# Kernel optimization log

Hardware: AMD Instinct MI355X
Metric: run time of the kernel (lower is better)

The kernel has to match this reference:

```python
import jax, jax.numpy as jnp
import numpy as np

N_NODES = 10000
IN_SIZE, H_SIZE, OUT_SIZE = 512, 512, 64
N_EDGES = 163840


def gcn_conv(x, edge_index, W, b, n_nodes):
    """PyG-style GCNConv: add self-loops, sym-normalize, x @ W, scatter-add, + bias."""
    src, dst = edge_index[0], edge_index[1]
    loop = jnp.arange(n_nodes, dtype=src.dtype)
    src = jnp.concatenate([src, loop])
    dst = jnp.concatenate([dst, loop])
    # degree over destinations (self-loops included)
    deg = jax.ops.segment_sum(jnp.ones_like(dst, dtype=x.dtype), dst, num_segments=n_nodes)
    dinv = jnp.where(deg > 0, jax.lax.rsqrt(deg), 0.0)
    norm = dinv[src] * dinv[dst]                      # [E+N]
    h = x @ W                                          # [N, out]
    msg = h[src] * norm[:, None]                       # gather + scale
    out = jax.ops.segment_sum(msg, dst, num_segments=n_nodes)  # scatter-add
    return out + b


def setup_inputs() -> dict:
    key = jax.random.key(0)
    k = jax.random.split(key, 6)
    x = jax.random.normal(k[0], (N_NODES, IN_SIZE), dtype=jnp.float32)
    edge_index = jax.random.randint(k[1], (2, N_EDGES), 0, N_NODES, dtype=jnp.int64 if jax.config.read('jax_enable_x64') else jnp.int32)
    # Glorot-ish init for weights, zero bias (PyG default)
    W1 = jax.random.normal(k[2], (IN_SIZE, H_SIZE), dtype=jnp.float32) * (1.0 / np.sqrt(IN_SIZE))
    b1 = jnp.zeros((H_SIZE,), dtype=jnp.float32)
    W2 = jax.random.normal(k[3], (H_SIZE, OUT_SIZE), dtype=jnp.float32) * (1.0 / np.sqrt(H_SIZE))
    b2 = jnp.zeros((OUT_SIZE,), dtype=jnp.float32)
    return {"x": x, "edge_index": edge_index, "W1": W1, "b1": b1, "W2": W2, "b2": b2}


def reference(x, edge_index, W1, b1, W2, b2):
    n = x.shape[0]
    h = gcn_conv(x, edge_index, W1, b1, n)
    h = jax.nn.relu(h)
    h = gcn_conv(h, edge_index, W2, b2, n)
    return (h, jax.nn.log_softmax(h, axis=1))
```

## Files before the change

kernel.cpp:

```cpp
#include <hip/hip_runtime.h>
#include <math.h>

#define NN 10000
#define INF 512
#define HF  512
#define OF  64
#define NE  163840
#define MAXDEG 64

typedef __attribute__((ext_vector_type(8))) short bf16x8_t;
typedef __attribute__((ext_vector_type(4))) float f32x4_t;

__device__ inline ushort f2bf(float f) {
    unsigned u = __float_as_uint(f);
    u = (u + 0x7FFF + ((u >> 16) & 1)) >> 16;
    return (ushort)u;
}
__device__ inline float bf2f(ushort u) {
    return __uint_as_float(((unsigned)u) << 16);
}

#define GLL(gp, lp) __builtin_amdgcn_global_load_lds(                         \
    (const __attribute__((address_space(1))) unsigned int*)(gp),              \
    (__attribute__((address_space(3))) unsigned int*)(lp), 16, 0, 0)

#define CCB_X  2500
#define CCB_W1 2756
#define CCB_W2 2788
#define CCB_Z  2828
__global__ __launch_bounds__(256) void k_cvt(const float* __restrict__ X,
                                             ushort* __restrict__ Xb,
                                             const float* __restrict__ W1,
                                             ushort* __restrict__ W1T,
                                             const float* __restrict__ W2,
                                             ushort* __restrict__ W2T,
                                             int* __restrict__ gdeg) {
    __shared__ float tl[32][33];
    int b = blockIdx.x, t = threadIdx.x;
    if (b < CCB_X) {
        int i = (b * 256 + t) * 2;
        const float4* Xv = (const float4*)X;
        float4 v0 = Xv[i], v1 = Xv[i + 1];
        ushort4 o0, o1;
        o0.x = f2bf(v0.x); o0.y = f2bf(v0.y); o0.z = f2bf(v0.z); o0.w = f2bf(v0.w);
        o1.x = f2bf(v1.x); o1.y = f2bf(v1.y); o1.z = f2bf(v1.z); o1.w = f2bf(v1.w);
        ((ushort4*)Xb)[i] = o0;
        ((ushort4*)Xb)[i + 1] = o1;
    } else if (b < CCB_W2) {
        const float* W; ushort* WT; int N, tile;
        if (b < CCB_W1) { W = W1; WT = W1T; N = 512; tile = b - CCB_X; }
        else            { W = W2; WT = W2T; N = 64;  tile = b - CCB_W1; }
        int k0 = (tile & 15) * 32;
        int n0 = (tile >> 4) * 32;
        int tx = t & 31, ty = t >> 5;
#pragma unroll
        for (int i = 0; i < 4; i++)
            tl[ty + i * 8][tx] = W[(size_t)(k0 + ty + i * 8) * N + n0 + tx];
        __syncthreads();
#pragma unroll
        for (int i = 0; i < 4; i++)
            WT[(size_t)(n0 + ty + i * 8) * 512 + k0 + tx] = f2bf(tl[tx][ty + i * 8]);
    } else {
        int i = (b - CCB_W2) * 256 + t;
        if (i < NN) gdeg[i] = 0;
    }
}

#define GEMM_B 316
__global__ __launch_bounds__(256) void k_gemm_ell(const ushort* __restrict__ Xb,
                                                  const ushort* __restrict__ WT,
                                                  ushort* __restrict__ Y,
                                                  const int* __restrict__ src,
                                                  const int* __restrict__ dst,
                                                  int* __restrict__ gdeg,
                                                  int* __restrict__ ell, int E) {
    __shared__ ushort As[128 * 64];
    __shared__ ushort Bs[128 * 64];
    int b = blockIdx.x;
    int tid = threadIdx.x;
    if (b >= GEMM_B) {
        int e = (b - GEMM_B) * 256 + tid;
        if (e < E) {
            int s = src[e], d = dst[e];
            int r = atomicAdd(&gdeg[d], 1);
            if (r < MAXDEG) ell[d * MAXDEG + r] = s;
        }
        return;
    }
    int lane = tid & 63;
    int wave = tid >> 6;
    int m = lane & 15;
    int q = lane >> 4;
    int m7 = m & 7;
    int wr = wave >> 1;
    int wc = wave & 1;
    int row0 = (b % 79) * 128;
    int col0 = (b / 79) * 128;

    int lrow = lane >> 3;
    int lg = ((lane & 7) ^ lrow) * 8;

    f32x4_t acc[4][4];
#pragma unroll
    for (int r = 0; r < 4; r++)
#pragma unroll
        for (int c = 0; c < 4; c++) acc[r][c] = (f32x4_t){0.f, 0.f, 0.f, 0.f};

    const ushort* gA0 = Xb + (size_t)(row0 + wave * 32 + lrow) * 512 + lg;
    const ushort* gB0 = WT + (size_t)(col0 + wave * 32 + lrow) * 512 + lg;
    ushort* lA0 = As + (wave * 32) * 64;
    ushort* lB0 = Bs + (wave * 32) * 64;

    for (int kb = 0; kb < 512; kb += 64) {
#pragma unroll
        for (int j = 0; j < 4; j++) {
            GLL(gA0 + kb + j * 8 * 512, lA0 + j * 8 * 64);
            GLL(gB0 + kb + j * 8 * 512, lB0 + j * 8 * 64);
        }
        __syncthreads();
#pragma unroll
        for (int kc = 0; kc < 2; kc++) {
            bf16x8_t a[4], bb[4];
            int slot = ((kc * 4 + q) ^ m7) * 8;
#pragma unroll
            for (int r = 0; r < 4; r++)
                a[r] = *(const bf16x8_t*)(As + (wr * 64 + r * 16 + m) * 64 + slot);
#pragma unroll
            for (int c = 0; c < 4; c++)
                bb[c] = *(const bf16x8_t*)(Bs + (wc * 64 + c * 16 + m) * 64 + slot);
#pragma unroll
            for (int r = 0; r < 4; r++)
#pragma unroll
                for (int c = 0; c < 4; c++)
                    acc[r][c] = __builtin_amdgcn_mfma_f32_16x16x32_bf16(a[r], bb[c], acc[r][c], 0, 0, 0);
        }
        __syncthreads();
    }
#pragma unroll
    for (int r = 0; r < 4; r++) {
#pragma unroll
        for (int c = 0; c < 4; c++) {
#pragma unroll
            for (int reg = 0; reg < 4; reg++) {
                int row = row0 + wr * 64 + r * 16 + q * 4 + reg;
                int col = col0 + wc * 64 + c * 16 + m;
                if (row < NN) Y[(size_t)row * 512 + col] = f2bf(acc[r][c][reg]);
            }
        }
    }
}

__global__ __launch_bounds__(256) void k_gemm64_mfma(const ushort* __restrict__ Ab,
                                                     const ushort* __restrict__ W2T,
                                                     ushort* __restrict__ Y) {
    __shared__ ushort As[64 * 64];
    __shared__ ushort Bs[64 * 64];
    int tid = threadIdx.x;
    int lane = tid & 63;
    int wave = tid >> 6;
    int m = lane & 15;
    int q = lane >> 4;
    int m7 = m & 7;
    int row0 = blockIdx.x * 64;

    int lrow = lane >> 3;
    int lg = ((lane & 7) ^ lrow) * 8;

    f32x4_t acc[4];
#pragma unroll
    for (int c = 0; c < 4; c++) acc[c] = (f32x4_t){0.f, 0.f, 0.f, 0.f};

    const ushort* gA0 = Ab + (size_t)(row0 + wave * 16 + lrow) * 512 + lg;
    const ushort* gB0 = W2T + (size_t)(wave * 16 + lrow) * 512 + lg;
    ushort* lA0 = As + (wave * 16) * 64;
    ushort* lB0 = Bs + (wave * 16) * 64;

    for (int kb = 0; kb < 512; kb += 64) {
#pragma unroll
        for (int j = 0; j < 2; j++) {
            GLL(gA0 + kb + j * 8 * 512, lA0 + j * 8 * 64);
            GLL(gB0 + kb + j * 8 * 512, lB0 + j * 8 * 64);
        }
        __syncthreads();
#pragma unroll
        for (int kc = 0; kc < 2; kc++) {
            int slot = ((kc * 4 + q) ^ m7) * 8;
            bf16x8_t a = *(const bf16x8_t*)(As + (wave * 16 + m) * 64 + slot);
#pragma unroll
            for (int c = 0; c < 4; c++) {
                bf16x8_t bfr = *(const bf16x8_t*)(Bs + (c * 16 + m) * 64 + slot);
                acc[c] = __builtin_amdgcn_mfma_f32_16x16x32_bf16(a, bfr, acc[c], 0, 0, 0);
            }
        }
        __syncthreads();
    }
#pragma unroll
    for (int c = 0; c < 4; c++) {
#pragma unroll
        for (int reg = 0; reg < 4; reg++) {
            int row = row0 + wave * 16 + q * 4 + reg;
            int col = c * 16 + m;
            if (row < NN) Y[(size_t)row * 64 + col] = f2bf(acc[c][reg]);
        }
    }
}

__global__ __launch_bounds__(64) void k_agg1(const ushort* __restrict__ h1b,
                                             const int* __restrict__ gdeg,
                                             const int* __restrict__ ell,
                                             const float* __restrict__ b,
                                             ushort* __restrict__ a1b) {
    __shared__ int   sidx[64];
    __shared__ float swt[64];
    int bid = blockIdx.x;
    int slice = bid & 3;
    int v = bid >> 2;
    int t = threadIdx.x;
    int fb = slice * 128 + t * 2;
    int deg = gdeg[v]; if (deg > MAXDEG) deg = MAXDEG;
    float dv = rsqrtf((float)(deg + 1));
    int s = 0; float wt = 0.f;
    if (t < deg) {
        s = ell[v * MAXDEG + t];
        wt = rsqrtf((float)(gdeg[s] + 1)) * dv;
    }
    sidx[t] = s; swt[t] = wt;
    __syncthreads();

    float ax[8], ay[8];
#pragma unroll
    for (int k = 0; k < 8; k++) { ax[k] = 0.f; ay[k] = 0.f; }
    {
        ushort2 u = *(const ushort2*)(h1b + (size_t)v * 512 + fb);
        float dv2 = dv * dv;
        ax[0] = bf2f(u.x) * dv2;
        ay[0] = bf2f(u.y) * dv2;
    }
    int nr = (deg + 7) & ~7;
    for (int i = 0; i < nr; i += 8) {
        int   sK[8]; float wK[8];
#pragma unroll
        for (int k = 0; k < 8; k++) { sK[k] = sidx[i + k]; wK[k] = swt[i + k]; }
#pragma unroll
        for (int k = 0; k < 8; k++) {
            ushort2 u = *(const ushort2*)(h1b + (size_t)sK[k] * 512 + fb);
            ax[k] += bf2f(u.x) * wK[k];
            ay[k] += bf2f(u.y) * wK[k];
        }
    }
    float tx = ((ax[0] + ax[1]) + (ax[2] + ax[3])) + ((ax[4] + ax[5]) + (ax[6] + ax[7]));
    float ty = ((ay[0] + ay[1]) + (ay[2] + ay[3])) + ((ay[4] + ay[5]) + (ay[6] + ay[7]));
    tx += b[fb];
    ty += b[fb + 1];
    ushort2 o;
    o.x = f2bf(tx > 0.f ? tx : 0.f);
    o.y = f2bf(ty > 0.f ? ty : 0.f);
    *(ushort2*)(a1b + (size_t)v * 512 + fb) = o;
}

__global__ __launch_bounds__(64) void k_agg2_lsm(const ushort* __restrict__ h2b,
                                                 const int* __restrict__ gdeg,
                                                 const int* __restrict__ ell,
                                                 const float* __restrict__ b,
                                                 float* __restrict__ out) {
    __shared__ int   sidx[64];
    __shared__ float swt[64];
    int v = blockIdx.x;
    int t = threadIdx.x;
    int deg = gdeg[v]; if (deg > MAXDEG) deg = MAXDEG;
    float dv = rsqrtf((float)(deg + 1));
    int s = 0; float wt = 0.f;
    if (t < deg) {
        s = ell[v * MAXDEG + t];
        wt = rsqrtf((float)(gdeg[s] + 1)) * dv;
    }
    sidx[t] = s; swt[t] = wt;
    __syncthreads();

    float acc[8];
#pragma unroll
    for (int k = 0; k < 8; k++) acc[k] = 0.f;
    acc[0] = bf2f(h2b[(size_t)v * 64 + t]) * (dv * dv);

    int nr = (deg + 7) & ~7;
    for (int i = 0; i < nr; i += 8) {
        int   sK[8]; float wK[8];
#pragma unroll
        for (int k = 0; k < 8; k++) { sK[k] = sidx[i + k]; wK[k] = swt[i + k]; }
#pragma unroll
        for (int k = 0; k < 8; k++)
            acc[k] += bf2f(h2b[(size_t)sK[k] * 64 + t]) * wK[k];
    }
    float h = ((acc[0] + acc[1]) + (acc[2] + acc[3])) +
              ((acc[4] + acc[5]) + (acc[6] + acc[7]));
    h += b[t];
    out[(size_t)v * 64 + t] = h;
    float m = h;
#pragma unroll
    for (int off = 32; off >= 1; off >>= 1) m = fmaxf(m, __shfl_xor(m, off, 64));
    float e = expf(h - m);
    float ssum = e;
#pragma unroll
    for (int off = 32; off >= 1; off >>= 1) ssum += __shfl_xor(ssum, off, 64);
    out[(size_t)NN * OF + (size_t)v * 64 + t] = h - m - logf(ssum);
}


extern "C" void kernel_launch(void* const* d_in, const int* in_sizes, int n_in,
                              void* d_out, int out_size, void* d_ws, size_t ws_size,
                              hipStream_t stream) {
    const float* x  = (const float*)d_in[0];
    const int*   ei = (const int*)d_in[1];
    const float* W1 = (const float*)d_in[2];
    const float* b1 = (const float*)d_in[3];
    const float* W2 = (const float*)d_in[4];
    const float* b2 = (const float*)d_in[5];
    float* out = (float*)d_out;

    int E = in_sizes[1] / 2;
    const int* src = ei;
    const int* dst = ei + E;

    char* w = (char*)d_ws;
    auto carve = [&](size_t bytes) {
        char* p = w;
        w += (bytes + 255) & ~size_t(255);
        return p;
    };
    ushort* Xb     = (ushort*)carve((size_t)NN * 512 * 2);
    ushort* h1b    = (ushort*)carve((size_t)NN * 512 * 2);
    ushort* a1b    = (ushort*)carve((size_t)NN * 512 * 2);
    ushort* h2b    = (ushort*)carve((size_t)NN * 64 * 2);
    ushort* W1Tb   = (ushort*)carve((size_t)512 * 512 * 2);
    ushort* W2Tb   = (ushort*)carve((size_t)64 * 512 * 2);
    int*   gdeg    = (int*)carve((size_t)NN * 4);
    int*   ell     = (int*)carve((size_t)NN * MAXDEG * 4);
    (void)ws_size;

    int fillB = (E + 255) / 256;
    k_cvt<<<CCB_Z, 256, 0, stream>>>(x, Xb, W1, W1Tb, W2, W2Tb, gdeg);
    k_gemm_ell<<<GEMM_B + fillB, 256, 0, stream>>>(Xb, W1Tb, h1b, src, dst,
                                                   gdeg, ell, E);
    k_agg1<<<NN * 4, 64, 0, stream>>>(h1b, gdeg, ell, b1, a1b);
    k_gemm64_mfma<<<(NN + 63) / 64, 256, 0, stream>>>(a1b, W2Tb, h2b);
    k_agg2_lsm<<<NN, 64, 0, stream>>>(h2b, gdeg, ell, b2, out);
}
```

Baseline: 131.4 us.

## Fuse layer-1 aggregation with layer-2 GEMM using split-K atomic accumulation

Replaces the separate agg1 and 64-wide GEMM kernels with one kernel. Each block gathers and aggregates 128 nodes over a 128-feature slice into LDS, applies bias and ReLU, then multiplies by the matching W2 slice with MFMA. The four slice partials are combined through fp32 atomicAdd into a buffer zeroed in the conversion kernel. This removes the a1 round trip through global memory and one launch. In exchange the gather runs on only 316 blocks with serial per-wave node loops, which reduces latency hiding, and layer-2 aggregation now reads fp32 instead of bf16.

```diff
diff --git a/kernel.cpp b/kernel.cpp
--- a/kernel.cpp
+++ b/kernel.cpp
@@ -28,13 +28,15 @@
 #define CCB_W1 2756
 #define CCB_W2 2788
 #define CCB_Z  2828
+#define CCB_H2 3453
 __global__ __launch_bounds__(256) void k_cvt(const float* __restrict__ X,
                                              ushort* __restrict__ Xb,
                                              const float* __restrict__ W1,
                                              ushort* __restrict__ W1T,
                                              const float* __restrict__ W2,
                                              ushort* __restrict__ W2T,
-                                             int* __restrict__ gdeg) {
+                                             int* __restrict__ gdeg,
+                                             float* __restrict__ h2f) {
     __shared__ float tl[32][33];
     int b = blockIdx.x, t = threadIdx.x;
     if (b < CCB_X) {
@@ -60,9 +62,12 @@
 #pragma unroll
         for (int i = 0; i < 4; i++)
             WT[(size_t)(n0 + ty + i * 8) * 512 + k0 + tx] = f2bf(tl[tx][ty + i * 8]);
-    } else {
+    } else if (b < CCB_Z) {
         int i = (b - CCB_W2) * 256 + t;
         if (i < NN) gdeg[i] = 0;
+    } else {
+        int i = (b - CCB_Z) * 256 + t;
+        ((float4*)h2f)[i] = make_float4(0.f, 0.f, 0.f, 0.f);
     }
 }
 
@@ -150,115 +155,115 @@
     }
 }
 
-__global__ __launch_bounds__(256) void k_gemm64_mfma(const ushort* __restrict__ Ab,
-                                                     const ushort* __restrict__ W2T,
-                                                     ushort* __restrict__ Y) {
-    __shared__ ushort As[64 * 64];
-    __shared__ ushort Bs[64 * 64];
+#define FUSE_B 316
+#define LDA2 136
+__global__ __launch_bounds__(256) void k_fuse(const ushort* __restrict__ h1b,
+                                              const int* __restrict__ gdeg,
+                                              const int* __restrict__ ell,
+                                              const float* __restrict__ b1,
+                                              const ushort* __restrict__ W2T,
+                                              float* __restrict__ h2f) {
+    __shared__ ushort a1s[128 * LDA2];
+    __shared__ ushort w2s[64 * LDA2];
+    int bid = blockIdx.x;
+    int slice = bid & 3;
+    int nt = bid >> 2;
     int tid = threadIdx.x;
     int lane = tid & 63;
-    int wave = tid >> 6;
-    int m = lane & 15;
-    int q = lane >> 4;
-    int m7 = m & 7;
-    int row0 = blockIdx.x * 64;
-
-    int lrow = lane >> 3;
-    int lg = ((lane & 7) ^ lrow) * 8;
-
-    f32x4_t acc[4];
-#pragma unroll
-    for (int c = 0; c < 4; c++) acc[c] = (f32x4_t){0.f, 0.f, 0.f, 0.f};
-
-    const ushort* gA0 = Ab + (size_t)(row0 + wave * 16 + lrow) * 512 + lg;
-    const ushort* gB0 = W2T + (size_t)(wave * 16 + lrow) * 512 + lg;
-    ushort* lA0 = As + (wave * 16) * 64;
-    ushort* lB0 = Bs + (wave * 16) * 64;
-
-    for (int kb = 0; kb < 512; kb += 64) {
-#pragma unroll
-        for (int j = 0; j < 2; j++) {
-            GLL(gA0 + kb + j * 8 * 512, lA0 + j * 8 * 64);
-            GLL(gB0 + kb + j * 8 * 512, lB0 + j * 8 * 64);
-        }
-        __syncthreads();
-#pragma unroll
-        for (int kc = 0; kc < 2; kc++) {
-            int slot = ((kc * 4 + q) ^ m7) * 8;
-            bf16x8_t a = *(const bf16x8_t*)(As + (wave * 16 + m) * 64 + slot);
-#pragma unroll
-            for (int c = 0; c < 4; c++) {
-                bf16x8_t bfr = *(const bf16x8_t*)(Bs + (c * 16 + m) * 64 + slot);
-                acc[c] = __builtin_amdgcn_mfma_f32_16x16x32_bf16(a, bfr, acc[c], 0, 0, 0);
-            }
-        }
-        __syncthreads();
-    }
-#pragma unroll
-    for (int c = 0; c < 4; c++) {
-#pragma unroll
-        for (int reg = 0; reg < 4; reg++) {
-            int row = row0 + wave * 16 + q * 4 + reg;
-            int col = c * 16 + m;
-            if (row < NN) Y[(size_t)row * 64 + col] = f2bf(acc[c][reg]);
-        }
-    }
-}
-
-__global__ __launch_bounds__(64) void k_agg1(const ushort* __restrict__ h1b,
-                                             const int* __restrict__ gdeg,
-                                             const int* __restrict__ ell,
-                                             const float* __restrict__ b,
-                                             ushort* __restrict__ a1b) {
-    __shared__ int   sidx[64];
-    __shared__ float swt[64];
-    int bid = blockIdx.x;
-    int slice = bid & 3;
-    int v = bid >> 2;
-    int t = threadIdx.x;
-    int fb = slice * 128 + t * 2;
-    int deg = gdeg[v]; if (deg > MAXDEG) deg = MAXDEG;
-    float dv = rsqrtf((float)(deg + 1));
-    int s = 0; float wt = 0.f;
-    if (t < deg) {
-        s = ell[v * MAXDEG + t];
-        wt = rsqrtf((float)(gdeg[s] + 1)) * dv;
-    }
-    sidx[t] = s; swt[t] = wt;
+    int wv = tid >> 6;
+
+    {
+        int row = tid >> 2, kq = (tid & 3) * 32;
+        const ushort* gsrc = W2T + (size_t)row * 512 + slice * 128 + kq;
+#pragma unroll
+        for (int j = 0; j < 4; j++)
+            *(bf16x8_t*)(w2s + row * LDA2 + kq + j * 8) = *(const bf16x8_t*)(gsrc + j * 8);
+    }
+
+    int fb = slice * 128 + lane * 2;
+    for (int i = 0; i < 32; i++) {
+        int n = nt * 128 + wv * 32 + i;
+        int nloc = wv * 32 + i;
+        float ax[8], ay[8];
+#pragma unroll
+        for (int k = 0; k < 8; k++) { ax[k] = 0.f; ay[k] = 0.f; }
+        int deg = 0;
+        int sreg = 0; float wreg = 0.f;
+        if (n < NN) {
+            int dt = gdeg[n];
+            deg = dt > MAXDEG ? MAXDEG : dt;
+            float dvn = rsqrtf((float)(dt + 1));
+            if (lane < deg) {
+                sreg = ell[n * MAXDEG + lane];
+                wreg = rsqrtf((float)(gdeg[sreg] + 1)) * dvn;
+            }
+            ushort2 u = *(const ushort2*)(h1b + (size_t)n * 512 + fb);
+            ax[0] = bf2f(u.x) * dvn * dvn;
+            ay[0] = bf2f(u.y) * dvn * dvn;
+        }
+        int nr = (deg + 7) & ~7;
+        for (int j = 0; j < nr; j += 8) {
+            int sK[8]; float wK[8];
+#pragma unroll
+            for (int k = 0; k < 8; k++) {
+                sK[k] = __shfl(sreg, j + k, 64);
+                wK[k] = __shfl(wreg, j + k, 64);
+            }
+#pragma unroll
+            for (int k = 0; k < 8; k++) {
+                ushort2 u = *(const ushort2*)(h1b + (size_t)sK[k] * 512 + fb);
+                ax[k] += bf2f(u.x) * wK[k];
+                ay[k] += bf2f(u.y) * wK[k];
+            }
+        }
+        float tx = ((ax[0] + ax[1]) + (ax[2] + ax[3])) + ((ax[4] + ax[5]) + (ax[6] + ax[7]));
+        float ty = ((ay[0] + ay[1]) + (ay[2] + ay[3])) + ((ay[4] + ay[5]) + (ay[6] + ay[7]));
+        tx += b1[fb];
+        ty += b1[fb + 1];
+        ushort2 o;
+        o.x = f2bf(tx > 0.f ? tx : 0.f);
+        o.y = f2bf(ty > 0.f ? ty : 0.f);
+        *(ushort2*)(a1s + nloc * LDA2 + lane * 2) = o;
+    }
     __syncthreads();
 
-    float ax[8], ay[8];
-#pragma unroll
-    for (int k = 0; k < 8; k++) { ax[k] = 0.f; ay[k] = 0.f; }
-    {
-        ushort2 u = *(const ushort2*)(h1b + (size_t)v * 512 + fb);
-        float dv2 = dv * dv;
-        ax[0] = bf2f(u.x) * dv2;
-        ay[0] = bf2f(u.y) * dv2;
-    }
-    int nr = (deg + 7) & ~7;
-    for (int i = 0; i < nr; i += 8) {
-        int   sK[8]; float wK[8];
-#pragma unroll
-        for (int k = 0; k < 8; k++) { sK[k] = sidx[i + k]; wK[k] = swt[i + k]; }
-#pragma unroll
-        for (int k = 0; k < 8; k++) {
-            ushort2 u = *(const ushort2*)(h1b + (size_t)sK[k] * 512 + fb);
-            ax[k] += bf2f(u.x) * wK[k];
-            ay[k] += bf2f(u.y) * wK[k];
-        }
-    }
-    float tx = ((ax[0] + ax[1]) + (ax[2] + ax[3])) + ((ax[4] + ax[5]) + (ax[6] + ax[7]));
-    float ty = ((ay[0] + ay[1]) + (ay[2] + ay[3])) + ((ay[4] + ay[5]) + (ay[6] + ay[7]));
-    tx += b[fb];
-    ty += b[fb + 1];
-    ushort2 o;
-    o.x = f2bf(tx > 0.f ? tx : 0.f);
-    o.y = f2bf(ty > 0.f ? ty : 0.f);
-    *(ushort2*)(a1b + (size_t)v * 512 + fb) = o;
-}
-
-__global__ __launch_bounds__(64) void k_agg2_lsm(const ushort* __restrict__ h2b,
+    int m = lane & 15, q = lane >> 4;
+    f32x4_t acc[2][4];
+#pragma unroll
+    for (int r = 0; r < 2; r++)
+#pragma unroll
+        for (int c = 0; c < 4; c++) acc[r][c] = (f32x4_t){0.f, 0.f, 0.f, 0.f};
+#pragma unroll
+    for (int kk = 0; kk < 4; kk++) {
+        int ko = kk * 32 + q * 8;
+        bf16x8_t a[2], bb[4];
+#pragma unroll
+        for (int r = 0; r < 2; r++)
+            a[r] = *(const bf16x8_t*)(a1s + (wv * 32 + r * 16 + m) * LDA2 + ko);
+#pragma unroll
+        for (int c = 0; c < 4; c++)
+            bb[c] = *(const bf16x8_t*)(w2s + (c * 16 + m) * LDA2 + ko);
+#pragma unroll
+        for (int r = 0; r < 2; r++)
+#pragma unroll
+            for (int c = 0; c < 4; c++)
+                acc[r][c] = __builtin_amdgcn_mfma_f32_16x16x32_bf16(a[r], bb[c], acc[r][c], 0, 0, 0);
+    }
+#pragma unroll
+    for (int r = 0; r < 2; r++) {
+#pragma unroll
+        for (int c = 0; c < 4; c++) {
+#pragma unroll
+            for (int reg = 0; reg < 4; reg++) {
+                int row = nt * 128 + wv * 32 + r * 16 + q * 4 + reg;
+                int col = c * 16 + m;
+                if (row < NN) atomicAdd(&h2f[(size_t)row * 64 + col], acc[r][c][reg]);
+            }
+        }
+    }
+}
+
+__global__ __launch_bounds__(64) void k_agg2_lsm(const float* __restrict__ h2f,
                                                  const int* __restrict__ gdeg,
                                                  const int* __restrict__ ell,
                                                  const float* __restrict__ b,
@@ -280,7 +285,7 @@
     float acc[8];
 #pragma unroll
     for (int k = 0; k < 8; k++) acc[k] = 0.f;
-    acc[0] = bf2f(h2b[(size_t)v * 64 + t]) * (dv * dv);
+    acc[0] = h2f[(size_t)v * 64 + t] * (dv * dv);
 
     int nr = (deg + 7) & ~7;
     for (int i = 0; i < nr; i += 8) {
@@ -289,7 +294,7 @@
         for (int k = 0; k < 8; k++) { sK[k] = sidx[i + k]; wK[k] = swt[i + k]; }
 #pragma unroll
         for (int k = 0; k < 8; k++)
-            acc[k] += bf2f(h2b[(size_t)sK[k] * 64 + t]) * wK[k];
+            acc[k] += h2f[(size_t)sK[k] * 64 + t] * wK[k];
     }
     float h = ((acc[0] + acc[1]) + (acc[2] + acc[3])) +
               ((acc[4] + acc[5]) + (acc[6] + acc[7]));
@@ -329,8 +334,7 @@
     };
     ushort* Xb     = (ushort*)carve((size_t)NN * 512 * 2);
     ushort* h1b    = (ushort*)carve((size_t)NN * 512 * 2);
-    ushort* a1b    = (ushort*)carve((size_t)NN * 512 * 2);
-    ushort* h2b    = (ushort*)carve((size_t)NN * 64 * 2);
+    float*  h2f    = (float*)carve((size_t)NN * 64 * 4);
     ushort* W1Tb   = (ushort*)carve((size_t)512 * 512 * 2);
     ushort* W2Tb   = (ushort*)carve((size_t)64 * 512 * 2);
     int*   gdeg    = (int*)carve((size_t)NN * 4);
@@ -338,10 +342,9 @@
     (void)ws_size;
 
     int fillB = (E + 255) / 256;
-    k_cvt<<<CCB_Z, 256, 0, stream>>>(x, Xb, W1, W1Tb, W2, W2Tb, gdeg);
+    k_cvt<<<CCB_H2, 256, 0, stream>>>(x, Xb, W1, W1Tb, W2, W2Tb, gdeg, h2f);
     k_gemm_ell<<<GEMM_B + fillB, 256, 0, stream>>>(Xb, W1Tb, h1b, src, dst,
                                                    gdeg, ell, E);
-    k_agg1<<<NN * 4, 64, 0, stream>>>(h1b, gdeg, ell, b1, a1b);
-    k_gemm64_mfma<<<(NN + 63) / 64, 256, 0, stream>>>(a1b, W2Tb, h2b);
-    k_agg2_lsm<<<NN, 64, 0, stream>>>(h2b, gdeg, ell, b2, out);
-}
+    k_fuse<<<FUSE_B, 256, 0, stream>>>(h1b, gdeg, ell, b1, W2Tb, h2f);
+    k_agg2_lsm<<<NN, 64, 0, stream>>>(h2f, gdeg, ell, b2, out);
+}
```

Result: slower. 175.1 us (+33.3%).
